# Kernel optimization log

Measured on AMD Instinct MI355X. Metric: run time of the kernel, lower is better.

The kernel has to match this reference:

```python
import jax, jax.numpy as jnp
import numpy as np

D_MODEL = 768
D_STATE = 16
D_CONV = 4
EXPAND = 2
D_IN = D_MODEL // 2          # per-direction model dim = 384
D_INNER = EXPAND * D_IN      # ssm inner dim = 768
DT_RANK = (D_IN + 15) // 16  # 24 (mamba 'auto')
B, L = 2, 2048
EPS = 1e-5


def silu(x):
    return x * jax.nn.sigmoid(x)


def layernorm(x, w, b):
    m = jnp.mean(x, axis=-1, keepdims=True)
    v = jnp.var(x, axis=-1, keepdims=True)
    return (x - m) * jax.lax.rsqrt(v + EPS) * w + b


def causal_conv1d(u, w, b):
    # u: (B,L,di), w: (di,K) depthwise causal conv, b: (di,)
    K = w.shape[1]
    up = jnp.pad(u, ((0, 0), (K - 1, 0), (0, 0)))
    Lq = u.shape[1]
    y = sum(up[:, k:k + Lq, :] * w[:, k] for k in range(K))
    return y + b


def mamba_ssm(u, in_w, in_b, conv_w, conv_b, xp_w, dt_w, dt_b, A_log, Dp, out_w, out_b):
    # u: (B,L,D_IN)
    Bz = u.shape[0]
    xz = u @ in_w + in_b                         # (B,L,2*D_INNER)
    x, z = jnp.split(xz, 2, axis=-1)             # (B,L,D_INNER) each
    x = silu(causal_conv1d(x, conv_w, conv_b))
    xd = x @ xp_w                                # (B,L,DT_RANK+2N)
    dt = jax.nn.softplus(xd[..., :DT_RANK] @ dt_w + dt_b)   # (B,L,D_INNER)
    Bm = xd[..., DT_RANK:DT_RANK + D_STATE]      # (B,L,N)
    Cm = xd[..., DT_RANK + D_STATE:]             # (B,L,N)
    A = -jnp.exp(A_log)                          # (D_INNER,N)

    def step(h, xs):
        dt_t, x_t, B_t, C_t = xs                 # (B,di),(B,di),(B,N),(B,N)
        h = jnp.exp(dt_t[..., None] * A) * h + (dt_t * x_t)[..., None] * B_t[:, None, :]
        y = jnp.einsum('bdn,bn->bd', h, C_t)
        return h, y

    h0 = jnp.zeros((Bz, D_INNER, D_STATE), x.dtype)
    xs = (dt.transpose(1, 0, 2), x.transpose(1, 0, 2),
          Bm.transpose(1, 0, 2), Cm.transpose(1, 0, 2))
    _, ys = jax.lax.scan(step, h0, xs)           # ys: (L,B,D_INNER)
    y = ys.transpose(1, 0, 2) + x * Dp
    y = y * silu(z)
    return y @ out_w + out_b                     # (B,L,D_IN)


def setup_inputs() -> dict:
    key = jax.random.key(0)

    def nrm(i, shape, s=0.02):
        return jax.random.normal(jax.random.fold_in(key, i), shape, jnp.float32) * s

    d = {"x": jax.random.normal(jax.random.fold_in(key, 0), (B, L, D_MODEL), jnp.float32)}
    d["in_norm_w"] = jnp.ones(D_MODEL); d["in_norm_b"] = jnp.zeros(D_MODEL)
    d["ip_w"] = nrm(1, (D_MODEL, 2 * D_IN)); d["ip_b"] = jnp.zeros(2 * D_IN)
    i = 10
    for p in ("f", "b"):
        d[p + "_in_w"] = nrm(i, (D_IN, 2 * D_INNER)); d[p + "_in_b"] = jnp.zeros(2 * D_INNER)
        d[p + "_conv_w"] = nrm(i + 1, (D_INNER, D_CONV), 0.2); d[p + "_conv_b"] = jnp.zeros(D_INNER)
        d[p + "_xp_w"] = nrm(i + 2, (D_INNER, DT_RANK + 2 * D_STATE))
        d[p + "_dt_w"] = nrm(i + 3, (DT_RANK, D_INNER), 0.1)
        d[p + "_dt_b"] = nrm(i + 4, (D_INNER,), 0.5)
        d[p + "_A_log"] = jnp.log(jnp.tile(jnp.arange(1, D_STATE + 1, dtype=jnp.float32), (D_INNER, 1)))
        d[p + "_D"] = jnp.ones(D_INNER)
        d[p + "_out_w"] = nrm(i + 5, (D_INNER, D_IN)); d[p + "_out_b"] = jnp.zeros(D_IN)
        i += 10
    d["op_w"] = nrm(30, (2 * D_IN, D_MODEL)); d["op_b"] = jnp.zeros(D_MODEL)
    d["norm_w"] = jnp.ones(D_MODEL); d["norm_b"] = jnp.zeros(D_MODEL)
    return d


def reference(x, in_norm_w, in_norm_b, ip_w, ip_b,
              f_in_w, f_in_b, f_conv_w, f_conv_b, f_xp_w, f_dt_w, f_dt_b, f_A_log, f_D, f_out_w, f_out_b,
              b_in_w, b_in_b, b_conv_w, b_conv_b, b_xp_w, b_dt_w, b_dt_b, b_A_log, b_D, b_out_w, b_out_b,
              op_w, op_b, norm_w, norm_b):
    residual = x
    xn = layernorm(x, in_norm_w, in_norm_b)
    xp = xn @ ip_w + ip_b                        # (B,L,2*D_IN)
    x_fwd, x_bwd = jnp.split(xp, 2, axis=-1)
    out_fwd = mamba_ssm(x_fwd, f_in_w, f_in_b, f_conv_w, f_conv_b, f_xp_w,
                        f_dt_w, f_dt_b, f_A_log, f_D, f_out_w, f_out_b)
    out_bwd = mamba_ssm(jnp.flip(x_bwd, axis=1), b_in_w, b_in_b, b_conv_w, b_conv_b, b_xp_w,
                        b_dt_w, b_dt_b, b_A_log, b_D, b_out_w, b_out_b)
    out_bwd = jnp.flip(out_bwd, axis=1)
    out = jnp.concatenate([out_fwd, out_bwd], axis=-1) @ op_w + op_b
    # dropout is identity in eval mode
    return layernorm(residual + out, norm_w, norm_b)
```

## Files before the change

### kernel.cpp

```cpp
#include <hip/hip_runtime.h>
#include <hip/hip_bf16.h>
#include <math.h>
#include <type_traits>

#define BATCH 2
#define SEQ   2048
#define DMODEL 768
#define DIN   384
#define DINNER 768
#define DSTATE 16
#define DTRANK 24
#define ROWS  (BATCH*SEQ)
#define NCH   32
#define CLEN  (SEQ/NCH)

using short8  = __attribute__((ext_vector_type(8))) short;
using floatx4 = __attribute__((ext_vector_type(4))) float;

__device__ __forceinline__ ushort f2bf(float f) {
    union { float f; uint u; } v; v.f = f;
    uint r = (v.u + 0x7fffu + ((v.u >> 16) & 1u)) >> 16;
    return (ushort)r;
}
__device__ __forceinline__ float bf2f(ushort h) {
    union { uint u; float f; } v; v.u = ((uint)h) << 16;
    return v.f;
}

__device__ __forceinline__ void async16(const ushort* g, ushort* l) {
    __builtin_amdgcn_global_load_lds(
        (const __attribute__((address_space(1))) void*)g,
        (__attribute__((address_space(3))) void*)l,
        16, 0, 0);
}

template<typename OUT>
__global__ __launch_bounds__(256) void ln_kernel(
    const float* __restrict__ x, const float* __restrict__ res,
    const float* __restrict__ w, const float* __restrict__ b,
    OUT* __restrict__ out)
{
    int row = blockIdx.x;
    int tid = threadIdx.x;
    const float* xr = x + (size_t)row * DMODEL;
    const float* rr = res ? res + (size_t)row * DMODEL : nullptr;
    float v[3];
    float s = 0.f, sq = 0.f;
#pragma unroll
    for (int j = 0; j < 3; j++) {
        int i = tid + j * 256;
        float val = xr[i];
        if (rr) val += rr[i];
        v[j] = val; s += val; sq += val * val;
    }
#pragma unroll
    for (int off = 32; off; off >>= 1) {
        s  += __shfl_down(s,  off);
        sq += __shfl_down(sq, off);
    }
    __shared__ float ss[4], ssq[4];
    __shared__ float mean_s, rstd_s;
    int wid = tid >> 6;
    if ((tid & 63) == 0) { ss[wid] = s; ssq[wid] = sq; }
    __syncthreads();
    if (tid == 0) {
        float S  = ss[0] + ss[1] + ss[2] + ss[3];
        float SQ = ssq[0] + ssq[1] + ssq[2] + ssq[3];
        float m  = S * (1.0f / DMODEL);
        float var = SQ * (1.0f / DMODEL) - m * m;
        mean_s = m;
        rstd_s = rsqrtf(var + 1e-5f);
    }
    __syncthreads();
    float m = mean_s, rs = rstd_s;
    OUT* orow = out + (size_t)row * DMODEL;
#pragma unroll
    for (int j = 0; j < 3; j++) {
        int i = tid + j * 256;
        float r = (v[j] - m) * rs * w[i] + b[i];
        if constexpr (std::is_same_v<OUT, ushort>) orow[i] = f2bf(r);
        else                                       orow[i] = r;
    }
}

struct TD { const float* src; ushort* dst; int K, N, Np, tile0, tk; };
struct TDs { TD d[8]; };

__global__ __launch_bounds__(256) void tcast_kernel(TDs ds)
{
    int bidx = blockIdx.x;
    int i = 0;
    while (i < 7 && bidx >= ds.d[i + 1].tile0) i++;
    TD t = ds.d[i];
    int local = bidx - t.tile0;
    int tk = local % t.tk, tn = local / t.tk;
    int tx = threadIdx.x & 31, ty = threadIdx.x >> 5;

    __shared__ float tile[32][33];
    int k0 = tk * 32, n0 = tn * 32;
#pragma unroll
    for (int r = ty; r < 32; r += 8) {
        int n = n0 + tx;
        tile[r][tx] = (n < t.N) ? t.src[(size_t)(k0 + r) * t.N + n] : 0.f;
    }
    __syncthreads();
#pragma unroll
    for (int r = ty; r < 32; r += 8) {
        int n = n0 + r, k = k0 + tx;
        t.dst[(size_t)n * t.K + k] = f2bf(tile[tx][r]);
    }
}

template<int TM, int TN, bool OUT_BF>
__global__ __launch_bounds__(256) void mfma_gemm(
    const ushort* __restrict__ A0, const ushort* __restrict__ A1, int lda,
    const ushort* __restrict__ B0, const ushort* __restrict__ B1, int ldb,
    const float* __restrict__ bias0, const float* __restrict__ bias1,
    void* __restrict__ C0, void* __restrict__ C1, int ldc, int N, int K)
{
    const ushort* A  = blockIdx.z ? A1 : A0;
    const ushort* Bt = blockIdx.z ? B1 : B0;
    const float* bias = blockIdx.z ? bias1 : bias0;
    void* Cout = blockIdx.z ? C1 : C0;

    constexpr int WM = TM / 2, WN = TN / 2;
    constexpr int MT = WM / 16, NT = WN / 16;
    __shared__ __align__(16) ushort lA[TM * 32];
    __shared__ __align__(16) ushort lB[TN * 32];
    const int tid = threadIdx.x;
    const int wave = tid >> 6, lane = tid & 63;
    const int wm = wave >> 1, wn = wave & 1;
    const int quad = lane >> 4, l16 = lane & 15;
    const int m0 = blockIdx.y * TM, n0 = blockIdx.x * TN;

    const int lrow = lane >> 2;
    const int lcol = (lane & 3) * 8;

    floatx4 acc[MT][NT];
#pragma unroll
    for (int i = 0; i < MT; i++)
#pragma unroll
        for (int j = 0; j < NT; j++)
            acc[i][j] = (floatx4){0.f, 0.f, 0.f, 0.f};

    constexpr int AI = TM / 64;
    constexpr int BI = TN / 64;

    for (int k0 = 0; k0 < K; k0 += 32) {
#pragma unroll
        for (int i = 0; i < AI; i++) {
            int rbase = (wave * AI + i) * 16;
            async16(A + (size_t)(m0 + rbase + lrow) * lda + k0 + lcol,
                    &lA[rbase * 32]);
        }
#pragma unroll
        for (int i = 0; i < BI; i++) {
            int rbase = (wave * BI + i) * 16;
            async16(Bt + (size_t)(n0 + rbase + lrow) * ldb + k0 + lcol,
                    &lB[rbase * 32]);
        }
        __syncthreads();
        short8 af[MT], bfr[NT];
#pragma unroll
        for (int i = 0; i < MT; i++)
            af[i] = *(const short8*)&lA[(wm * WM + i * 16 + l16) * 32 + quad * 8];
#pragma unroll
        for (int j = 0; j < NT; j++)
            bfr[j] = *(const short8*)&lB[(wn * WN + j * 16 + l16) * 32 + quad * 8];
#pragma unroll
        for (int i = 0; i < MT; i++)
#pragma unroll
            for (int j = 0; j < NT; j++)
                acc[i][j] = __builtin_amdgcn_mfma_f32_16x16x32_bf16(af[i], bfr[j], acc[i][j], 0, 0, 0);
        __syncthreads();
    }
#pragma unroll
    for (int i = 0; i < MT; i++) {
#pragma unroll
        for (int j = 0; j < NT; j++) {
            int row = m0 + wm * WM + i * 16 + quad * 4;
            int col = n0 + wn * WN + j * 16 + l16;
            if (col < N) {
                float bv = bias ? bias[col] : 0.f;
#pragma unroll
                for (int r = 0; r < 4; r++) {
                    float v = acc[i][j][r] + bv;
                    if (OUT_BF) ((ushort*)Cout)[(size_t)(row + r) * ldc + col] = f2bf(v);
                    else        ((float*)Cout)[(size_t)(row + r) * ldc + col] = v;
                }
            }
        }
    }
}

#define BM 64
#define BN 64
#define BK 16
__global__ __launch_bounds__(256) void dt_gemm_kernel(
    const float* __restrict__ A0f, const float* __restrict__ A1f, int lda,
    const float* __restrict__ W0, const float* __restrict__ W1, int ldw,
    const float* __restrict__ bias0, const float* __restrict__ bias1,
    float* __restrict__ C0f, float* __restrict__ C1f, int ldc,
    int M, int N, int K)
{
    const float* A = blockIdx.z ? A1f : A0f;
    const float* W = blockIdx.z ? W1 : W0;
    const float* bias = blockIdx.z ? bias1 : bias0;
    float* C = blockIdx.z ? C1f : C0f;

    __shared__ float As[BK][BM + 4];
    __shared__ float Bs[BK][BN + 4];
    int tid = threadIdx.x;
    int m0 = blockIdx.y * BM;
    int n0 = blockIdx.x * BN;
    int tx = tid & 15, ty = tid >> 4;
    float acc[4][4] = {};

    for (int k0 = 0; k0 < K; k0 += BK) {
        {
            int row = tid >> 2;
            int kq  = (tid & 3) * 4;
            const float* ap = A + (size_t)(m0 + row) * lda + k0 + kq;
            float4 av;
            if (k0 + BK <= K) {
                av = *(const float4*)ap;
            } else {
                float t0 = (k0 + kq + 0 < K) ? ap[0] : 0.f;
                float t1 = (k0 + kq + 1 < K) ? ap[1] : 0.f;
                float t2 = (k0 + kq + 2 < K) ? ap[2] : 0.f;
                float t3 = (k0 + kq + 3 < K) ? ap[3] : 0.f;
                av = make_float4(t0, t1, t2, t3);
            }
            As[kq + 0][row] = av.x;
            As[kq + 1][row] = av.y;
            As[kq + 2][row] = av.z;
            As[kq + 3][row] = av.w;
        }
        {
            int krow = tid >> 4;
            int col  = (tid & 15) * 4;
            float4 wv = make_float4(0.f, 0.f, 0.f, 0.f);
            if (k0 + krow < K) {
                const float* wp = W + (size_t)(k0 + krow) * ldw + n0 + col;
                wv = *(const float4*)wp;
            }
            *(float4*)&Bs[krow][col] = wv;
        }
        __syncthreads();
#pragma unroll
        for (int k = 0; k < BK; k++) {
            float a[4], bv[4];
            *(float4*)a  = *(const float4*)&As[k][ty * 4];
            *(float4*)bv = *(const float4*)&Bs[k][tx * 4];
#pragma unroll
            for (int i = 0; i < 4; i++)
#pragma unroll
                for (int j = 0; j < 4; j++)
                    acc[i][j] = fmaf(a[i], bv[j], acc[i][j]);
        }
        __syncthreads();
    }
#pragma unroll
    for (int i = 0; i < 4; i++) {
        int m = m0 + ty * 4 + i;
#pragma unroll
        for (int j = 0; j < 4; j++) {
            int n = n0 + tx * 4 + j;
            float v = acc[i][j] + bias[n];
            v = (v > 20.f) ? v : log1pf(__expf(v));
            C[(size_t)m * ldc + n] = v;
        }
    }
}

__global__ __launch_bounds__(256) void conv_silu_kernel(
    const ushort* __restrict__ xzf, const ushort* __restrict__ xzb,
    const float* __restrict__ cwf, const float* __restrict__ cbf,
    const float* __restrict__ cwb, const float* __restrict__ cbb,
    ushort* __restrict__ outf, ushort* __restrict__ outb)
{
    int rev = blockIdx.y;
    const ushort* xz = rev ? xzb : xzf;
    const float* cw = rev ? cwb : cwf;
    const float* cb = rev ? cbb : cbf;
    ushort* out = rev ? outb : outf;

    int idx = blockIdx.x * 256 + threadIdx.x;
    int d = idx % DINNER;
    int row = idx / DINNER;
    int t = row & (SEQ - 1);
    int b = row >> 11;
    float acc = cb[d];
#pragma unroll
    for (int k = 0; k < 4; k++) {
        int ts = rev ? (t + 3 - k) : (t - 3 + k);
        if (ts >= 0 && ts < SEQ)
            acc = fmaf(cw[d * 4 + k], bf2f(xz[((size_t)(b * SEQ + ts)) * 1536 + d]), acc);
    }
    float sig = 1.f / (1.f + __expf(-acc));
    out[idx] = f2bf(acc * sig);
}

template<bool FULL>
__global__ __launch_bounds__(256) void scan_chunk_kernel(
    const float* __restrict__ dtf, const ushort* __restrict__ xcf,
    const float* __restrict__ xdf, const ushort* __restrict__ xzf,
    const float* __restrict__ Alf, const float* __restrict__ Dff,
    const float* __restrict__ dtb, const ushort* __restrict__ xcb,
    const float* __restrict__ xdb, const ushort* __restrict__ xzb,
    const float* __restrict__ Alb, const float* __restrict__ Dbb,
    float* __restrict__ Hloc, float* __restrict__ Wp,
    const float* __restrict__ Hin,
    ushort* __restrict__ yf, ushort* __restrict__ yb)
{
    const int d     = blockIdx.x * 256 + threadIdx.x;
    const int chunk = blockIdx.y;
    const int bz    = blockIdx.z;
    const int dir   = bz >> 1;
    const int bat   = bz & 1;

    const float*  dt = dir ? dtb : dtf;
    const ushort* xc = dir ? xcb : xcf;
    const float*  xd = dir ? xdb : xdf;
    const ushort* xz = dir ? xzb : xzf;
    const float*  Al = dir ? Alb : Alf;
    const float*  Dp = dir ? Dbb : Dff;
    ushort* yo = dir ? yb : yf;

    float a[16];
    {
        const float4* Ap = (const float4*)(Al + (size_t)d * 16);
#pragma unroll
        for (int q = 0; q < 4; q++) {
            float4 v = Ap[q];
            a[q*4+0] = -__expf(v.x); a[q*4+1] = -__expf(v.y);
            a[q*4+2] = -__expf(v.z); a[q*4+3] = -__expf(v.w);
        }
    }
    const float a0 = a[0];
    bool fast = true;
#pragma unroll
    for (int n = 0; n < 16; n++) {
        float ideal = a0 * (float)(n + 1);
        fast = fast && (fabsf(a[n] - ideal) <= 1e-4f * fabsf(ideal) + 1e-7f);
    }

    float h[16];
    if (FULL) {
        size_t base = ((size_t)(bz * NCH + chunk) * DINNER + d) * 16;
        const float4* hp = (const float4*)(Hin + base);
#pragma unroll
        for (int q = 0; q < 4; q++) {
            float4 v = hp[q];
            h[q*4+0] = v.x; h[q*4+1] = v.y; h[q*4+2] = v.z; h[q*4+3] = v.w;
        }
    } else {
#pragma unroll
        for (int n = 0; n < 16; n++) h[n] = 0.f;
    }

    const float Dd = FULL ? Dp[d] : 0.f;
    float S = 0.f;

    auto run = [&](auto FASTC) {
        constexpr bool FAST = decltype(FASTC)::value;
#pragma unroll 2
        for (int i = 0; i < CLEN; i++) {
            int tl = chunk * CLEN + i;
            int t  = dir ? (SEQ - 1 - tl) : tl;
            size_t r = (size_t)(bat * SEQ + t);
            float dtv = dt[r * DINNER + d];
            float xv  = bf2f(xc[r * DINNER + d]);
            const float* bp = xd + r * 56 + DTRANK;
            float4 B0 = *(const float4*)(bp + 0);
            float4 B1 = *(const float4*)(bp + 4);
            float4 B2 = *(const float4*)(bp + 8);
            float4 B3 = *(const float4*)(bp + 12);
            float Bv[16] = {B0.x,B0.y,B0.z,B0.w, B1.x,B1.y,B1.z,B1.w,
                            B2.x,B2.y,B2.z,B2.w, B3.x,B3.y,B3.z,B3.w};
            float w[16];
            if (FAST) {
                float e1 = __expf(dtv * a0);
                float e2 = e1*e1, e4 = e2*e2, e8 = e4*e4;
                w[0]=e1;      w[1]=e2;      w[2]=e2*e1;   w[3]=e4;
                w[4]=e4*e1;   w[5]=e4*e2;   w[6]=e4*w[2]; w[7]=e8;
                w[8]=e8*e1;   w[9]=e8*e2;   w[10]=e8*w[2];w[11]=e8*e4;
                w[12]=e8*w[4];w[13]=e8*w[5];w[14]=e8*w[6];w[15]=e8*e8;
            } else {
#pragma unroll
                for (int n = 0; n < 16; n++) w[n] = __expf(dtv * a[n]);
            }
            float bx = dtv * xv;
#pragma unroll
            for (int n = 0; n < 16; n++)
                h[n] = fmaf(w[n], h[n], bx * Bv[n]);
            S += dtv;
            if (FULL) {
                const float* cp = bp + DSTATE;
                float4 C0 = *(const float4*)(cp + 0);
                float4 C1 = *(const float4*)(cp + 4);
                float4 C2 = *(const float4*)(cp + 8);
                float4 C3 = *(const float4*)(cp + 12);
                float Cv[16] = {C0.x,C0.y,C0.z,C0.w, C1.x,C1.y,C1.z,C1.w,
                                C2.x,C2.y,C2.z,C2.w, C3.x,C3.y,C3.z,C3.w};
                float y = 0.f;
#pragma unroll
                for (int n = 0; n < 16; n++) y = fmaf(h[n], Cv[n], y);
                float zv = bf2f(xz[r * 1536 + DINNER + d]);
                float sig = 1.f / (1.f + __expf(-zv));
                yo[r * DINNER + d] = f2bf((y + xv * Dd) * (zv * sig));
            }
        }
    };
    if (fast) run(std::true_type{}); else run(std::false_type{});

    if (!FULL) {
        float W[16];
        if (fast) {
            float E1 = __expf(S * a0);
            float E2 = E1*E1, E4 = E2*E2, E8 = E4*E4;
            W[0]=E1;      W[1]=E2;      W[2]=E2*E1;   W[3]=E4;
            W[4]=E4*E1;   W[5]=E4*E2;   W[6]=E4*W[2]; W[7]=E8;
            W[8]=E8*E1;   W[9]=E8*E2;   W[10]=E8*W[2];W[11]=E8*E4;
            W[12]=E8*W[4];W[13]=E8*W[5];W[14]=E8*W[6];W[15]=E8*E8;
        } else {
#pragma unroll
            for (int n = 0; n < 16; n++) W[n] = __expf(S * a[n]);
        }
        size_t base = ((size_t)(bz * NCH + chunk) * DINNER + d) * 16;
#pragma unroll
        for (int q = 0; q < 4; q++) {
            *(float4*)(Hloc + base + q*4) = make_float4(h[q*4+0], h[q*4+1], h[q*4+2], h[q*4+3]);
            *(float4*)(Wp   + base + q*4) = make_float4(W[q*4+0], W[q*4+1], W[q*4+2], W[q*4+3]);
        }
    }
}

__global__ __launch_bounds__(256) void scan_combine(
    const float* __restrict__ Hloc, const float* __restrict__ Wp,
    float* __restrict__ Hin)
{
    int idx = blockIdx.x * 256 + threadIdx.x;
    int bz = idx / (DINNER * 16);
    int rest = idx % (DINNER * 16);
    float hin = 0.f;
#pragma unroll
    for (int k = 0; k < NCH; k++) {
        size_t o = (size_t)(bz * NCH + k) * (DINNER * 16) + rest;
        Hin[o] = hin;
        hin = fmaf(Wp[o], hin, Hloc[o]);
    }
}

extern "C" void kernel_launch(void* const* d_in, const int* in_sizes, int n_in,
                              void* d_out, int out_size, void* d_ws, size_t ws_size,
                              hipStream_t stream)
{
    const float* x        = (const float*)d_in[0];
    const float* in_nw    = (const float*)d_in[1];
    const float* in_nb    = (const float*)d_in[2];
    const float* ip_w     = (const float*)d_in[3];
    const float* ip_b     = (const float*)d_in[4];
    const float* f_in_w   = (const float*)d_in[5];
    const float* f_in_b   = (const float*)d_in[6];
    const float* f_conv_w = (const float*)d_in[7];
    const float* f_conv_b = (const float*)d_in[8];
    const float* f_xp_w   = (const float*)d_in[9];
    const float* f_dt_w   = (const float*)d_in[10];
    const float* f_dt_b   = (const float*)d_in[11];
    const float* f_A_log  = (const float*)d_in[12];
    const float* f_D      = (const float*)d_in[13];
    const float* f_out_w  = (const float*)d_in[14];
    const float* f_out_b  = (const float*)d_in[15];
    const float* b_in_w   = (const float*)d_in[16];
    const float* b_in_b   = (const float*)d_in[17];
    const float* b_conv_w = (const float*)d_in[18];
    const float* b_conv_b = (const float*)d_in[19];
    const float* b_xp_w   = (const float*)d_in[20];
    const float* b_dt_w   = (const float*)d_in[21];
    const float* b_dt_b   = (const float*)d_in[22];
    const float* b_A_log  = (const float*)d_in[23];
    const float* b_D      = (const float*)d_in[24];
    const float* b_out_w  = (const float*)d_in[25];
    const float* b_out_b  = (const float*)d_in[26];
    const float* op_w     = (const float*)d_in[27];
    const float* op_b     = (const float*)d_in[28];
    const float* norm_w   = (const float*)d_in[29];
    const float* norm_b   = (const float*)d_in[30];

    size_t off = 0;
    auto alloc = [&](size_t bytes) {
        void* p = (char*)d_ws + off;
        off += (bytes + 255) & ~(size_t)255;
        return p;
    };
    const size_t R = ROWS;
    ushort* xn_bf   = (ushort*)alloc(R * 768 * 2);
    ushort* xp_bf   = (ushort*)alloc(R * 768 * 2);
    ushort* xz_f_bf = (ushort*)alloc(R * 1536 * 2);
    ushort* xz_b_bf = (ushort*)alloc(R * 1536 * 2);
    ushort* xc_f_bf = (ushort*)alloc(R * 768 * 2);
    ushort* xc_b_bf = (ushort*)alloc(R * 768 * 2);
    float*  xd_f    = (float*)alloc(R * 56 * 4);
    float*  xd_b    = (float*)alloc(R * 56 * 4);
    float*  dt_f    = (float*)alloc(R * 768 * 4);
    float*  dt_b    = (float*)alloc(R * 768 * 4);
    ushort* y_f_bf  = (ushort*)alloc(R * 768 * 2);
    ushort* y_b_bf  = (ushort*)alloc(R * 768 * 2);
    ushort* cat_bf  = (ushort*)alloc(R * 768 * 2);
    float*  outraw  = (float*)alloc(R * 768 * 4);
    const size_t SCN = (size_t)4 * NCH * DINNER * 16;
    float* Hloc = (float*)alloc(SCN * 4);
    float* Wpb  = (float*)alloc(SCN * 4);
    float* Hin  = (float*)alloc(SCN * 4);
    ushort* Wt_ip   = (ushort*)alloc((size_t)768 * 768 * 2);
    ushort* Wt_fin  = (ushort*)alloc((size_t)1536 * 384 * 2);
    ushort* Wt_bin  = (ushort*)alloc((size_t)1536 * 384 * 2);
    ushort* Wt_fxp  = (ushort*)alloc((size_t)64 * 768 * 2);
    ushort* Wt_bxp  = (ushort*)alloc((size_t)64 * 768 * 2);
    ushort* Wt_fout = (ushort*)alloc((size_t)384 * 768 * 2);
    ushort* Wt_bout = (ushort*)alloc((size_t)384 * 768 * 2);
    ushort* Wt_op   = (ushort*)alloc((size_t)768 * 768 * 2);

    dim3 blk(256);

    TDs td;
    int tile0 = 0, nd = 0;
    auto add = [&](const float* s, ushort* dst, int K, int N, int Np) {
        td.d[nd] = TD{s, dst, K, N, Np, tile0, K / 32};
        tile0 += (K / 32) * (Np / 32);
        nd++;
    };
    add(ip_w,    Wt_ip,   768, 768, 768);
    add(f_in_w,  Wt_fin,  384, 1536, 1536);
    add(b_in_w,  Wt_bin,  384, 1536, 1536);
    add(f_xp_w,  Wt_fxp,  768, 56, 64);
    add(b_xp_w,  Wt_bxp,  768, 56, 64);
    add(f_out_w, Wt_fout, 768, 384, 384);
    add(b_out_w, Wt_bout, 768, 384, 384);
    add(op_w,    Wt_op,   768, 768, 768);
    hipLaunchKernelGGL(tcast_kernel, dim3(tile0), blk, 0, stream, td);

    hipLaunchKernelGGL((ln_kernel<ushort>), dim3(ROWS), blk, 0, stream,
                       x, (const float*)nullptr, in_nw, in_nb, xn_bf);
    hipLaunchKernelGGL((mfma_gemm<128,64,true>), dim3(768/64, ROWS/128, 1), blk, 0, stream,
                       xn_bf, xn_bf, 768, Wt_ip, Wt_ip, 768, ip_b, ip_b,
                       (void*)xp_bf, (void*)xp_bf, 768, 768, 768);
    hipLaunchKernelGGL((mfma_gemm<128,128,true>), dim3(1536/128, ROWS/128, 2), blk, 0, stream,
                       xp_bf, xp_bf + 384, 768, Wt_fin, Wt_bin, 384,
                       f_in_b, b_in_b, (void*)xz_f_bf, (void*)xz_b_bf, 1536, 1536, 384);
    hipLaunchKernelGGL(conv_silu_kernel, dim3(ROWS * DINNER / 256, 2), blk, 0, stream,
                       xz_f_bf, xz_b_bf, f_conv_w, f_conv_b, b_conv_w, b_conv_b,
                       xc_f_bf, xc_b_bf);
    hipLaunchKernelGGL((mfma_gemm<64,64,false>), dim3(1, ROWS/64, 2), blk, 0, stream,
                       xc_f_bf, xc_b_bf, 768, Wt_fxp, Wt_bxp, 768,
                       (const float*)nullptr, (const float*)nullptr,
                       (void*)xd_f, (void*)xd_b, 56, 56, 768);
    hipLaunchKernelGGL(dt_gemm_kernel, dim3(768 / BN, ROWS / BM, 2), blk, 0, stream,
                       xd_f, xd_b, 56, f_dt_w, b_dt_w, 768, f_dt_b, b_dt_b,
                       dt_f, dt_b, 768, ROWS, 768, DTRANK);
    hipLaunchKernelGGL((scan_chunk_kernel<false>), dim3(DINNER / 256, NCH, 4), blk, 0, stream,
                       dt_f, xc_f_bf, xd_f, xz_f_bf, f_A_log, f_D,
                       dt_b, xc_b_bf, xd_b, xz_b_bf, b_A_log, b_D,
                       Hloc, Wpb, (const float*)nullptr, (ushort*)nullptr, (ushort*)nullptr);
    hipLaunchKernelGGL(scan_combine, dim3(4 * DINNER * 16 / 256), blk, 0, stream,
                       Hloc, Wpb, Hin);
    hipLaunchKernelGGL((scan_chunk_kernel<true>), dim3(DINNER / 256, NCH, 4), blk, 0, stream,
                       dt_f, xc_f_bf, xd_f, xz_f_bf, f_A_log, f_D,
                       dt_b, xc_b_bf, xd_b, xz_b_bf, b_A_log, b_D,
                       (float*)nullptr, (float*)nullptr, Hin, y_f_bf, y_b_bf);
    hipLaunchKernelGGL((mfma_gemm<128,64,true>), dim3(384/64, ROWS/128, 2), blk, 0, stream,
                       y_f_bf, y_b_bf, 768, Wt_fout, Wt_bout, 768,
                       f_out_b, b_out_b, (void*)cat_bf, (void*)(cat_bf + 384), 768, 384, 768);
    hipLaunchKernelGGL((mfma_gemm<128,64,false>), dim3(768/64, ROWS/128, 1), blk, 0, stream,
                       cat_bf, cat_bf, 768, Wt_op, Wt_op, 768, op_b, op_b,
                       (void*)outraw, (void*)outraw, 768, 768, 768);
    hipLaunchKernelGGL((ln_kernel<float>), dim3(ROWS), blk, 0, stream,
                       x, outraw, norm_w, norm_b, (float*)d_out);
}
```

Baseline: 352.3 us.

## Fold adjacent linear projections into fused weights and merge prep kernels

Precomputes combined weights by multiplying ip_w into the in_proj weights and the out_proj weights into op_w, with matching fused biases. The separate xp and cat GEMMs disappear and activations pass through fewer full-size matmuls and intermediate buffers. It also merges weight casting with the input layernorm into one launch, doubles the GEMM K-step to 64, vectorises the conv kernel to 8 channels per thread, and doubles the scan chunk count. The per-call weight-fusion GEMMs add cost, and rounding the fused weights to bf16 changes numerics slightly.

```diff
diff --git a/kernel.cpp b/kernel.cpp
--- a/kernel.cpp
+++ b/kernel.cpp
@@ -11,7 +11,7 @@
 #define DSTATE 16
 #define DTRANK 24
 #define ROWS  (BATCH*SEQ)
-#define NCH   32
+#define NCH   64
 #define CLEN  (SEQ/NCH)
 
 using short8  = __attribute__((ext_vector_type(8))) short;
@@ -26,7 +26,6 @@
     union { uint u; float f; } v; v.u = ((uint)h) << 16;
     return v.f;
 }
-
 __device__ __forceinline__ void async16(const ushort* g, ushort* l) {
     __builtin_amdgcn_global_load_lds(
         (const __attribute__((address_space(1))) void*)g,
@@ -34,13 +33,136 @@
         16, 0, 0);
 }
 
-template<typename OUT>
-__global__ __launch_bounds__(256) void ln_kernel(
-    const float* __restrict__ x, const float* __restrict__ res,
+template<int TM, int TN> struct GemmShT { ushort lA[TM * 64]; ushort lB[TN * 64]; };
+
+template<int TM, int TN>
+__device__ __forceinline__ void gemm_accum(
+    const ushort* __restrict__ A, int lda,
+    const ushort* __restrict__ Bt, int ldb,
+    int K, int m0, int n0, GemmShT<TM, TN>& sh,
+    floatx4 (&acc)[TM / 32][TN / 32])
+{
+    constexpr int WM = TM / 2, WN = TN / 2;
+    constexpr int MT = WM / 16, NT = WN / 16;
+    constexpr int AI = TM / 32, BI = TN / 32;
+    const int tid = threadIdx.x;
+    const int wave = tid >> 6, lane = tid & 63;
+    const int wm = wave >> 1, wn = wave & 1;
+    const int quad = lane >> 4, l16 = lane & 15;
+    const int lrow = lane >> 3, lcol = (lane & 7) * 8;
+
+    for (int k0 = 0; k0 < K; k0 += 64) {
+#pragma unroll
+        for (int i = 0; i < AI; i++) {
+            int rb = (wave * AI + i) * 8;
+            async16(A + (size_t)(m0 + rb + lrow) * lda + k0 + lcol, &sh.lA[rb * 64]);
+        }
+#pragma unroll
+        for (int i = 0; i < BI; i++) {
+            int rb = (wave * BI + i) * 8;
+            async16(Bt + (size_t)(n0 + rb + lrow) * ldb + k0 + lcol, &sh.lB[rb * 64]);
+        }
+        __syncthreads();
+#pragma unroll
+        for (int ks = 0; ks < 2; ks++) {
+            short8 af[MT], bf[NT];
+#pragma unroll
+            for (int i = 0; i < MT; i++)
+                af[i] = *(const short8*)&sh.lA[(wm * WM + i * 16 + l16) * 64 + ks * 32 + quad * 8];
+#pragma unroll
+            for (int j = 0; j < NT; j++)
+                bf[j] = *(const short8*)&sh.lB[(wn * WN + j * 16 + l16) * 64 + ks * 32 + quad * 8];
+#pragma unroll
+            for (int i = 0; i < MT; i++)
+#pragma unroll
+                for (int j = 0; j < NT; j++)
+                    acc[i][j] = __builtin_amdgcn_mfma_f32_16x16x32_bf16(af[i], bf[j], acc[i][j], 0, 0, 0);
+        }
+        __syncthreads();
+    }
+}
+
+template<int TM, int TN, bool OUT_BF>
+__device__ __forceinline__ void gemm_epilogue(
+    const float* __restrict__ bias, void* __restrict__ C, int ldc, int N,
+    int m0, int n0, floatx4 (&acc)[TM / 32][TN / 32])
+{
+    constexpr int WM = TM / 2, WN = TN / 2;
+    constexpr int MT = WM / 16, NT = WN / 16;
+    const int tid = threadIdx.x;
+    const int wave = tid >> 6, lane = tid & 63;
+    const int wm = wave >> 1, wn = wave & 1;
+    const int quad = lane >> 4, l16 = lane & 15;
+#pragma unroll
+    for (int i = 0; i < MT; i++) {
+#pragma unroll
+        for (int j = 0; j < NT; j++) {
+            int row = m0 + wm * WM + i * 16 + quad * 4;
+            int col = n0 + wn * WN + j * 16 + l16;
+            if (col < N) {
+                float bv = bias ? bias[col] : 0.f;
+#pragma unroll
+                for (int r = 0; r < 4; r++) {
+                    float v = acc[i][j][r] + bv;
+                    if (OUT_BF) ((ushort*)C)[(size_t)(row + r) * ldc + col] = f2bf(v);
+                    else        ((float*)C)[(size_t)(row + r) * ldc + col] = v;
+                }
+            }
+        }
+    }
+}
+
+template<int TM, int TN, bool OUT_BF>
+__global__ __launch_bounds__(256) void mfma_gemm_k(
+    const ushort* __restrict__ A0, const ushort* __restrict__ A1, int lda,
+    const ushort* __restrict__ B0, const ushort* __restrict__ B1, int ldb,
+    const float* __restrict__ bias0, const float* __restrict__ bias1,
+    void* __restrict__ C0, void* __restrict__ C1, int ldc, int N, int K)
+{
+    __shared__ GemmShT<TM, TN> sh;
+    const ushort* A  = blockIdx.z ? A1 : A0;
+    const ushort* Bt = blockIdx.z ? B1 : B0;
+    const float* bias = blockIdx.z ? bias1 : bias0;
+    void* C = blockIdx.z ? C1 : C0;
+    floatx4 acc[TM / 32][TN / 32];
+#pragma unroll
+    for (int i = 0; i < TM / 32; i++)
+#pragma unroll
+        for (int j = 0; j < TN / 32; j++)
+            acc[i][j] = (floatx4){0.f, 0.f, 0.f, 0.f};
+    int m0 = blockIdx.y * TM, n0 = blockIdx.x * TN;
+    gemm_accum<TM, TN>(A, lda, Bt, ldb, K, m0, n0, sh, acc);
+    gemm_epilogue<TM, TN, OUT_BF>(bias, C, ldc, N, m0, n0, acc);
+}
+
+template<int TM, int TN>
+__global__ __launch_bounds__(256) void outop_kernel(
+    const ushort* __restrict__ A0, const ushort* __restrict__ B0,
+    const ushort* __restrict__ A1, const ushort* __restrict__ B1,
+    const float* __restrict__ bias, float* __restrict__ C,
+    int lda, int ldb, int ldc, int N, int K)
+{
+    __shared__ GemmShT<TM, TN> sh;
+    floatx4 acc[TM / 32][TN / 32];
+#pragma unroll
+    for (int i = 0; i < TM / 32; i++)
+#pragma unroll
+        for (int j = 0; j < TN / 32; j++)
+            acc[i][j] = (floatx4){0.f, 0.f, 0.f, 0.f};
+    int m0 = blockIdx.y * TM, n0 = blockIdx.x * TN;
+    gemm_accum<TM, TN>(A0, lda, B0, ldb, K, m0, n0, sh, acc);
+    gemm_accum<TM, TN>(A1, lda, B1, ldb, K, m0, n0, sh, acc);
+    gemm_epilogue<TM, TN, false>(bias, (void*)C, ldc, N, m0, n0, acc);
+}
+
+struct LnSh { float ss[4]; float ssq[4]; float m; float rs; };
+
+template<bool OUT_BF>
+__device__ __forceinline__ void ln_row(
+    int row, const float* __restrict__ x, const float* __restrict__ res,
     const float* __restrict__ w, const float* __restrict__ b,
-    OUT* __restrict__ out)
-{
-    int row = blockIdx.x;
+    void* __restrict__ out, LnSh& sh)
+{
     int tid = threadIdx.x;
     const float* xr = x + (size_t)row * DMODEL;
     const float* rr = res ? res + (size_t)row * DMODEL : nullptr;
@@ -58,139 +180,169 @@
         s  += __shfl_down(s,  off);
         sq += __shfl_down(sq, off);
     }
-    __shared__ float ss[4], ssq[4];
-    __shared__ float mean_s, rstd_s;
     int wid = tid >> 6;
-    if ((tid & 63) == 0) { ss[wid] = s; ssq[wid] = sq; }
+    if ((tid & 63) == 0) { sh.ss[wid] = s; sh.ssq[wid] = sq; }
     __syncthreads();
     if (tid == 0) {
-        float S  = ss[0] + ss[1] + ss[2] + ss[3];
-        float SQ = ssq[0] + ssq[1] + ssq[2] + ssq[3];
+        float S  = sh.ss[0] + sh.ss[1] + sh.ss[2] + sh.ss[3];
+        float SQ = sh.ssq[0] + sh.ssq[1] + sh.ssq[2] + sh.ssq[3];
         float m  = S * (1.0f / DMODEL);
         float var = SQ * (1.0f / DMODEL) - m * m;
-        mean_s = m;
-        rstd_s = rsqrtf(var + 1e-5f);
+        sh.m = m;
+        sh.rs = rsqrtf(var + 1e-5f);
     }
     __syncthreads();
-    float m = mean_s, rs = rstd_s;
-    OUT* orow = out + (size_t)row * DMODEL;
+    float m = sh.m, rs = sh.rs;
 #pragma unroll
     for (int j = 0; j < 3; j++) {
         int i = tid + j * 256;
         float r = (v[j] - m) * rs * w[i] + b[i];
-        if constexpr (std::is_same_v<OUT, ushort>) orow[i] = f2bf(r);
-        else                                       orow[i] = r;
-    }
-}
-
-struct TD { const float* src; ushort* dst; int K, N, Np, tile0, tk; };
-struct TDs { TD d[8]; };
-
-__global__ __launch_bounds__(256) void tcast_kernel(TDs ds)
-{
-    int bidx = blockIdx.x;
-    int i = 0;
-    while (i < 7 && bidx >= ds.d[i + 1].tile0) i++;
-    TD t = ds.d[i];
-    int local = bidx - t.tile0;
-    int tk = local % t.tk, tn = local / t.tk;
-    int tx = threadIdx.x & 31, ty = threadIdx.x >> 5;
-
-    __shared__ float tile[32][33];
-    int k0 = tk * 32, n0 = tn * 32;
-#pragma unroll
-    for (int r = ty; r < 32; r += 8) {
-        int n = n0 + tx;
-        tile[r][tx] = (n < t.N) ? t.src[(size_t)(k0 + r) * t.N + n] : 0.f;
-    }
-    __syncthreads();
-#pragma unroll
-    for (int r = ty; r < 32; r += 8) {
-        int n = n0 + r, k = k0 + tx;
-        t.dst[(size_t)n * t.K + k] = f2bf(tile[tx][r]);
-    }
-}
-
-template<int TM, int TN, bool OUT_BF>
-__global__ __launch_bounds__(256) void mfma_gemm(
-    const ushort* __restrict__ A0, const ushort* __restrict__ A1, int lda,
-    const ushort* __restrict__ B0, const ushort* __restrict__ B1, int ldb,
-    const float* __restrict__ bias0, const float* __restrict__ bias1,
-    void* __restrict__ C0, void* __restrict__ C1, int ldc, int N, int K)
-{
-    const ushort* A  = blockIdx.z ? A1 : A0;
-    const ushort* Bt = blockIdx.z ? B1 : B0;
-    const float* bias = blockIdx.z ? bias1 : bias0;
-    void* Cout = blockIdx.z ? C1 : C0;
-
-    constexpr int WM = TM / 2, WN = TN / 2;
-    constexpr int MT = WM / 16, NT = WN / 16;
-    __shared__ __align__(16) ushort lA[TM * 32];
-    __shared__ __align__(16) ushort lB[TN * 32];
-    const int tid = threadIdx.x;
-    const int wave = tid >> 6, lane = tid & 63;
-    const int wm = wave >> 1, wn = wave & 1;
-    const int quad = lane >> 4, l16 = lane & 15;
-    const int m0 = blockIdx.y * TM, n0 = blockIdx.x * TN;
-
-    const int lrow = lane >> 2;
-    const int lcol = (lane & 3) * 8;
-
-    floatx4 acc[MT][NT];
-#pragma unroll
-    for (int i = 0; i < MT; i++)
-#pragma unroll
-        for (int j = 0; j < NT; j++)
-            acc[i][j] = (floatx4){0.f, 0.f, 0.f, 0.f};
-
-    constexpr int AI = TM / 64;
-    constexpr int BI = TN / 64;
-
-    for (int k0 = 0; k0 < K; k0 += 32) {
-#pragma unroll
-        for (int i = 0; i < AI; i++) {
-            int rbase = (wave * AI + i) * 16;
-            async16(A + (size_t)(m0 + rbase + lrow) * lda + k0 + lcol,
-                    &lA[rbase * 32]);
-        }
-#pragma unroll
-        for (int i = 0; i < BI; i++) {
-            int rbase = (wave * BI + i) * 16;
-            async16(Bt + (size_t)(n0 + rbase + lrow) * ldb + k0 + lcol,
-                    &lB[rbase * 32]);
-        }
-        __syncthreads();
-        short8 af[MT], bfr[NT];
-#pragma unroll
-        for (int i = 0; i < MT; i++)
-            af[i] = *(const short8*)&lA[(wm * WM + i * 16 + l16) * 32 + quad * 8];
-#pragma unroll
-        for (int j = 0; j < NT; j++)
-            bfr[j] = *(const short8*)&lB[(wn * WN + j * 16 + l16) * 32 + quad * 8];
-#pragma unroll
-        for (int i = 0; i < MT; i++)
-#pragma unroll
-            for (int j = 0; j < NT; j++)
-                acc[i][j] = __builtin_amdgcn_mfma_f32_16x16x32_bf16(af[i], bfr[j], acc[i][j], 0, 0, 0);
-        __syncthreads();
-    }
-#pragma unroll
-    for (int i = 0; i < MT; i++) {
-#pragma unroll
-        for (int j = 0; j < NT; j++) {
-            int row = m0 + wm * WM + i * 16 + quad * 4;
-            int col = n0 + wn * WN + j * 16 + l16;
-            if (col < N) {
-                float bv = bias ? bias[col] : 0.f;
-#pragma unroll
-                for (int r = 0; r < 4; r++) {
-                    float v = acc[i][j][r] + bv;
-                    if (OUT_BF) ((ushort*)Cout)[(size_t)(row + r) * ldc + col] = f2bf(v);
-                    else        ((float*)Cout)[(size_t)(row + r) * ldc + col] = v;
-                }
+        if (OUT_BF) ((ushort*)out)[(size_t)row * DMODEL + i] = f2bf(r);
+        else        ((float*)out)[(size_t)row * DMODEL + i] = r;
+    }
+}
+
+__global__ __launch_bounds__(256) void ln2_kernel(
+    const float* __restrict__ x, const float* __restrict__ res,
+    const float* __restrict__ w, const float* __restrict__ b,
+    float* __restrict__ out)
+{
+    __shared__ LnSh sh;
+    ln_row<false>(blockIdx.x, x, res, w, b, (void*)out, sh);
+}
+
+struct TD { const float* src; ushort* dst; int K, N, Np, tile0, tk, mode; };
+struct PrepArgs {
+    TD d[8];
+    int ntc;
+    const float *x, *in_nw, *in_nb;
+    ushort* xn;
+};
+
+__global__ __launch_bounds__(256) void prep_kernel(PrepArgs p)
+{
+    __shared__ union { float tile[32][33]; LnSh l; } sh;
+    int bi = blockIdx.x;
+    if (bi < p.ntc) {
+        int i = 0;
+        while (i < 7 && bi >= p.d[i + 1].tile0) i++;
+        TD t = p.d[i];
+        int local = bi - t.tile0;
+        int tki = local % t.tk, tn = local / t.tk;
+        int k0 = tki * 32, n0 = tn * 32;
+        if (t.mode == 0) {
+            int tx = threadIdx.x & 31, ty = threadIdx.x >> 5;
+#pragma unroll
+            for (int r = ty; r < 32; r += 8) {
+                int n = n0 + tx;
+                sh.tile[r][tx] = (n < t.N) ? t.src[(size_t)(k0 + r) * t.N + n] : 0.f;
             }
-        }
-    }
+            __syncthreads();
+#pragma unroll
+            for (int r = ty; r < 32; r += 8) {
+                int n = n0 + r, k = k0 + tx;
+                t.dst[(size_t)n * t.K + k] = f2bf(sh.tile[tx][r]);
+            }
+        } else {
+#pragma unroll
+            for (int e = threadIdx.x; e < 1024; e += 256) {
+                int r = e >> 5, c = e & 31;
+                size_t o = (size_t)(k0 + r) * t.N + n0 + c;
+                t.dst[o] = f2bf(t.src[o]);
+            }
+        }
+    } else {
+        ln_row<true>(bi - p.ntc, p.x, (const float*)nullptr, p.in_nw, p.in_nb,
+                     (void*)p.xn, sh.l);
+    }
+}
+
+struct WfArgs {
+    const ushort *fin, *bin, *opT, *ipc, *fow, *bow;
+    ushort *WzF, *WzB, *WoF, *WoB;
+    const float *ip_b, *f_in_b, *b_in_b, *f_out_b, *b_out_b, *op_b;
+    const float *f_in_w32, *b_in_w32, *op_w32;
+    float *bzf, *bzb, *bo;
+};
+
+__global__ __launch_bounds__(256) void wfuse_kernel(WfArgs p)
+{
+    __shared__ GemmShT<128, 64> sh;
+    int t = blockIdx.x;
+    if (t < 432) {
+        const ushort *A, *Bt; ushort* C; int lda, ldb, m0, n0;
+        if (t < 144)      { A = p.fin;       lda = 384; Bt = p.ipc;       ldb = 768; C = p.WzF; int u = t;       m0 = (u / 12) * 128; n0 = (u % 12) * 64; }
+        else if (t < 288) { A = p.bin;       lda = 384; Bt = p.ipc + 384; ldb = 768; C = p.WzB; int u = t - 144; m0 = (u / 12) * 128; n0 = (u % 12) * 64; }
+        else if (t < 360) { A = p.opT;       lda = 768; Bt = p.fow;       ldb = 384; C = p.WoF; int u = t - 288; m0 = (u / 12) * 128; n0 = (u % 12) * 64; }
+        else              { A = p.opT + 384; lda = 768; Bt = p.bow;       ldb = 384; C = p.WoB; int u = t - 360; m0 = (u / 12) * 128; n0 = (u % 12) * 64; }
+        floatx4 acc[4][2];
+#pragma unroll
+        for (int i = 0; i < 4; i++)
+#pragma unroll
+            for (int j = 0; j < 2; j++)
+                acc[i][j] = (floatx4){0.f, 0.f, 0.f, 0.f};
+        gemm_accum<128, 64>(A, lda, Bt, ldb, 384, m0, n0, sh, acc);
+        gemm_epilogue<128, 64, true>((const float*)nullptr, (void*)C, 768, 768, m0, n0, acc);
+    } else if (t < 438) {
+        int n = (t - 432) * 256 + threadIdx.x;
+        float acc = p.f_in_b[n];
+        for (int j = 0; j < 384; j++)
+            acc = fmaf(p.ip_b[j], p.f_in_w32[(size_t)j * 1536 + n], acc);
+        p.bzf[n] = acc;
+    } else if (t < 444) {
+        int n = (t - 438) * 256 + threadIdx.x;
+        float acc = p.b_in_b[n];
+        for (int j = 0; j < 384; j++)
+            acc = fmaf(p.ip_b[384 + j], p.b_in_w32[(size_t)j * 1536 + n], acc);
+        p.bzb[n] = acc;
+    } else {
+        int n = (t - 444) * 256 + threadIdx.x;
+        float acc = p.op_b[n];
+        for (int j = 0; j < 384; j++)
+            acc = fmaf(p.f_out_b[j], p.op_w32[(size_t)j * 768 + n], acc);
+        for (int j = 0; j < 384; j++)
+            acc = fmaf(p.b_out_b[j], p.op_w32[(size_t)(384 + j) * 768 + n], acc);
+        p.bo[n] = acc;
+    }
+}
+
+__global__ __launch_bounds__(256) void conv_silu_kernel(
+    const ushort* __restrict__ xzf, const ushort* __restrict__ xzb,
+    const float* __restrict__ cwf, const float* __restrict__ cbf,
+    const float* __restrict__ cwb, const float* __restrict__ cbb,
+    ushort* __restrict__ outf, ushort* __restrict__ outb)
+{
+    int rev = blockIdx.y;
+    const ushort* xz = rev ? xzb : xzf;
+    const float* cw = rev ? cwb : cwf;
+    const float* cb = rev ? cbb : cbf;
+    ushort* out = rev ? outb : outf;
+
+    int idx = blockIdx.x * 256 + threadIdx.x;
+    int dg = idx % (DINNER / 8);
+    int row = idx / (DINNER / 8);
+    int d0 = dg * 8;
+    int t = row & (SEQ - 1), b = row >> 11;
+    float acc[8];
+#pragma unroll
+    for (int c = 0; c < 8; c++) acc[c] = cb[d0 + c];
+#pragma unroll
+    for (int k = 0; k < 4; k++) {
+        int ts = rev ? (t + 3 - k) : (t - 3 + k);
+        if (ts >= 0 && ts < SEQ) {
+            short8 v = *(const short8*)&xz[((size_t)(b * SEQ + ts)) * 1536 + d0];
+#pragma unroll
+            for (int c = 0; c < 8; c++)
+                acc[c] = fmaf(cw[(d0 + c) * 4 + k], bf2f((ushort)v[c]), acc[c]);
+        }
+    }
+    short8 o;
+#pragma unroll
+    for (int c = 0; c < 8; c++) {
+        float sig = 1.f / (1.f + __expf(-acc[c]));
+        o[c] = (short)f2bf(acc[c] * sig);
+    }
+    *(short8*)&out[(size_t)row * DINNER + d0] = o;
 }
 
 #define BM 64
@@ -200,8 +352,7 @@
     const float* __restrict__ A0f, const float* __restrict__ A1f, int lda,
     const float* __restrict__ W0, const float* __restrict__ W1, int ldw,
     const float* __restrict__ bias0, const float* __restrict__ bias1,
-    float* __restrict__ C0f, float* __restrict__ C1f, int ldc,
-    int M, int N, int K)
+    float* __restrict__ C0f, float* __restrict__ C1f, int ldc, int K)
 {
     const float* A = blockIdx.z ? A1f : A0f;
     const float* W = blockIdx.z ? W1 : W0;
@@ -221,29 +372,17 @@
             int row = tid >> 2;
             int kq  = (tid & 3) * 4;
             const float* ap = A + (size_t)(m0 + row) * lda + k0 + kq;
-            float4 av;
-            if (k0 + BK <= K) {
-                av = *(const float4*)ap;
-            } else {
-                float t0 = (k0 + kq + 0 < K) ? ap[0] : 0.f;
-                float t1 = (k0 + kq + 1 < K) ? ap[1] : 0.f;
-                float t2 = (k0 + kq + 2 < K) ? ap[2] : 0.f;
-                float t3 = (k0 + kq + 3 < K) ? ap[3] : 0.f;
-                av = make_float4(t0, t1, t2, t3);
-            }
-            As[kq + 0][row] = av.x;
-            As[kq + 1][row] = av.y;
-            As[kq + 2][row] = av.z;
-            As[kq + 3][row] = av.w;
+            As[kq + 0][row] = (k0 + kq + 0 < K) ? ap[0] : 0.f;
+            As[kq + 1][row] = (k0 + kq + 1 < K) ? ap[1] : 0.f;
+            As[kq + 2][row] = (k0 + kq + 2 < K) ? ap[2] : 0.f;
+            As[kq + 3][row] = (k0 + kq + 3 < K) ? ap[3] : 0.f;
         }
         {
             int krow = tid >> 4;
             int col  = (tid & 15) * 4;
             float4 wv = make_float4(0.f, 0.f, 0.f, 0.f);
-            if (k0 + krow < K) {
-                const float* wp = W + (size_t)(k0 + krow) * ldw + n0 + col;
-                wv = *(const float4*)wp;
-            }
+            if (k0 + krow < K)
+                wv = *(const float4*)(W + (size_t)(k0 + krow) * ldw + n0 + col);
             *(float4*)&Bs[krow][col] = wv;
         }
         __syncthreads();
@@ -271,34 +410,6 @@
             C[(size_t)m * ldc + n] = v;
         }
     }
-}
-
-__global__ __launch_bounds__(256) void conv_silu_kernel(
-    const ushort* __restrict__ xzf, const ushort* __restrict__ xzb,
-    const float* __restrict__ cwf, const float* __restrict__ cbf,
-    const float* __restrict__ cwb, const float* __restrict__ cbb,
-    ushort* __restrict__ outf, ushort* __restrict__ outb)
-{
-    int rev = blockIdx.y;
-    const ushort* xz = rev ? xzb : xzf;
-    const float* cw = rev ? cwb : cwf;
-    const float* cb = rev ? cbb : cbf;
-    ushort* out = rev ? outb : outf;
-
-    int idx = blockIdx.x * 256 + threadIdx.x;
-    int d = idx % DINNER;
-    int row = idx / DINNER;
-    int t = row & (SEQ - 1);
-    int b = row >> 11;
-    float acc = cb[d];
-#pragma unroll
-    for (int k = 0; k < 4; k++) {
-        int ts = rev ? (t + 3 - k) : (t - 3 + k);
-        if (ts >= 0 && ts < SEQ)
-            acc = fmaf(cw[d * 4 + k], bf2f(xz[((size_t)(b * SEQ + ts)) * 1536 + d]), acc);
-    }
-    float sig = 1.f / (1.f + __expf(-acc));
-    out[idx] = f2bf(acc * sig);
 }
 
 template<bool FULL>
@@ -348,10 +459,9 @@
     float h[16];
     if (FULL) {
         size_t base = ((size_t)(bz * NCH + chunk) * DINNER + d) * 16;
-        const float4* hp = (const float4*)(Hin + base);
 #pragma unroll
         for (int q = 0; q < 4; q++) {
-            float4 v = hp[q];
+            float4 v = *(const float4*)(Hin + base + q * 4);
             h[q*4+0] = v.x; h[q*4+1] = v.y; h[q*4+2] = v.z; h[q*4+3] = v.w;
         }
     } else {
@@ -444,7 +554,7 @@
     int bz = idx / (DINNER * 16);
     int rest = idx % (DINNER * 16);
     float hin = 0.f;
-#pragma unroll
+#pragma unroll 4
     for (int k = 0; k < NCH; k++) {
         size_t o = (size_t)(bz * NCH + k) * (DINNER * 16) + rest;
         Hin[o] = hin;
@@ -496,7 +606,6 @@
     };
     const size_t R = ROWS;
     ushort* xn_bf   = (ushort*)alloc(R * 768 * 2);
-    ushort* xp_bf   = (ushort*)alloc(R * 768 * 2);
     ushort* xz_f_bf = (ushort*)alloc(R * 1536 * 2);
     ushort* xz_b_bf = (ushort*)alloc(R * 1536 * 2);
     ushort* xc_f_bf = (ushort*)alloc(R * 768 * 2);
@@ -507,74 +616,88 @@
     float*  dt_b    = (float*)alloc(R * 768 * 4);
     ushort* y_f_bf  = (ushort*)alloc(R * 768 * 2);
     ushort* y_b_bf  = (ushort*)alloc(R * 768 * 2);
-    ushort* cat_bf  = (ushort*)alloc(R * 768 * 2);
     float*  outraw  = (float*)alloc(R * 768 * 4);
     const size_t SCN = (size_t)4 * NCH * DINNER * 16;
     float* Hloc = (float*)alloc(SCN * 4);
     float* Wpb  = (float*)alloc(SCN * 4);
     float* Hin  = (float*)alloc(SCN * 4);
-    ushort* Wt_ip   = (ushort*)alloc((size_t)768 * 768 * 2);
-    ushort* Wt_fin  = (ushort*)alloc((size_t)1536 * 384 * 2);
-    ushort* Wt_bin  = (ushort*)alloc((size_t)1536 * 384 * 2);
-    ushort* Wt_fxp  = (ushort*)alloc((size_t)64 * 768 * 2);
-    ushort* Wt_bxp  = (ushort*)alloc((size_t)64 * 768 * 2);
-    ushort* Wt_fout = (ushort*)alloc((size_t)384 * 768 * 2);
-    ushort* Wt_bout = (ushort*)alloc((size_t)384 * 768 * 2);
-    ushort* Wt_op   = (ushort*)alloc((size_t)768 * 768 * 2);
-
-    dim3 blk(256);
-
-    TDs td;
+    ushort* Wt_fin = (ushort*)alloc((size_t)1536 * 384 * 2);
+    ushort* Wt_bin = (ushort*)alloc((size_t)1536 * 384 * 2);
+    ushort* Wt_op  = (ushort*)alloc((size_t)768 * 768 * 2);
+    ushort* Wt_fxp = (ushort*)alloc((size_t)64 * 768 * 2);
+    ushort* Wt_bxp = (ushort*)alloc((size_t)64 * 768 * 2);
+    ushort* ipc    = (ushort*)alloc((size_t)768 * 768 * 2);
+    ushort* fow    = (ushort*)alloc((size_t)768 * 384 * 2);
+    ushort* bow    = (ushort*)alloc((size_t)768 * 384 * 2);
+    ushort* WzF    = (ushort*)alloc((size_t)1536 * 768 * 2);
+    ushort* WzB    = (ushort*)alloc((size_t)1536 * 768 * 2);
+    ushort* WoF    = (ushort*)alloc((size_t)768 * 768 * 2);
+    ushort* WoB    = (ushort*)alloc((size_t)768 * 768 * 2);
+    float*  bzf    = (float*)alloc(1536 * 4);
+    float*  bzb    = (float*)alloc(1536 * 4);
+    float*  bo     = (float*)alloc(768 * 4);
+
+    PrepArgs pa;
     int tile0 = 0, nd = 0;
-    auto add = [&](const float* s, ushort* dst, int K, int N, int Np) {
-        td.d[nd] = TD{s, dst, K, N, Np, tile0, K / 32};
-        tile0 += (K / 32) * (Np / 32);
+    auto add = [&](const float* s, ushort* dst, int K, int N, int Np, int mode) {
+        int tiles = mode == 0 ? (K / 32) * (Np / 32) : (K / 32) * (N / 32);
+        pa.d[nd] = TD{s, dst, K, N, Np, tile0, K / 32, mode};
+        tile0 += tiles;
         nd++;
     };
-    add(ip_w,    Wt_ip,   768, 768, 768);
-    add(f_in_w,  Wt_fin,  384, 1536, 1536);
-    add(b_in_w,  Wt_bin,  384, 1536, 1536);
-    add(f_xp_w,  Wt_fxp,  768, 56, 64);
-    add(b_xp_w,  Wt_bxp,  768, 56, 64);
-    add(f_out_w, Wt_fout, 768, 384, 384);
-    add(b_out_w, Wt_bout, 768, 384, 384);
-    add(op_w,    Wt_op,   768, 768, 768);
-    hipLaunchKernelGGL(tcast_kernel, dim3(tile0), blk, 0, stream, td);
-
-    hipLaunchKernelGGL((ln_kernel<ushort>), dim3(ROWS), blk, 0, stream,
-                       x, (const float*)nullptr, in_nw, in_nb, xn_bf);
-    hipLaunchKernelGGL((mfma_gemm<128,64,true>), dim3(768/64, ROWS/128, 1), blk, 0, stream,
-                       xn_bf, xn_bf, 768, Wt_ip, Wt_ip, 768, ip_b, ip_b,
-                       (void*)xp_bf, (void*)xp_bf, 768, 768, 768);
-    hipLaunchKernelGGL((mfma_gemm<128,128,true>), dim3(1536/128, ROWS/128, 2), blk, 0, stream,
-                       xp_bf, xp_bf + 384, 768, Wt_fin, Wt_bin, 384,
-                       f_in_b, b_in_b, (void*)xz_f_bf, (void*)xz_b_bf, 1536, 1536, 384);
-    hipLaunchKernelGGL(conv_silu_kernel, dim3(ROWS * DINNER / 256, 2), blk, 0, stream,
+    add(f_in_w,  Wt_fin, 384, 1536, 1536, 0);
+    add(b_in_w,  Wt_bin, 384, 1536, 1536, 0);
+    add(op_w,    Wt_op,  768, 768, 768, 0);
+    add(f_xp_w,  Wt_fxp, 768, 56, 64, 0);
+    add(b_xp_w,  Wt_bxp, 768, 56, 64, 0);
+    add(ip_w,    ipc,    768, 768, 768, 1);
+    add(f_out_w, fow,    768, 384, 384, 1);
+    add(b_out_w, bow,    768, 384, 384, 1);
+    pa.ntc = tile0;
+    pa.x = x; pa.in_nw = in_nw; pa.in_nb = in_nb; pa.xn = xn_bf;
+    hipLaunchKernelGGL(prep_kernel, dim3(tile0 + ROWS), dim3(256), 0, stream, pa);
+
+    WfArgs wa;
+    wa.fin = Wt_fin; wa.bin = Wt_bin; wa.opT = Wt_op;
+    wa.ipc = ipc; wa.fow = fow; wa.bow = bow;
+    wa.WzF = WzF; wa.WzB = WzB; wa.WoF = WoF; wa.WoB = WoB;
+    wa.ip_b = ip_b; wa.f_in_b = f_in_b; wa.b_in_b = b_in_b;
+    wa.f_out_b = f_out_b; wa.b_out_b = b_out_b; wa.op_b = op_b;
+    wa.f_in_w32 = f_in_w; wa.b_in_w32 = b_in_w; wa.op_w32 = op_w;
+    wa.bzf = bzf; wa.bzb = bzb; wa.bo = bo;
+    hipLaunchKernelGGL(wfuse_kernel, dim3(447), dim3(256), 0, stream, wa);
+
+    hipLaunchKernelGGL((mfma_gemm_k<128, 128, true>), dim3(12, 32, 2), dim3(256), 0, stream,
+                       xn_bf, xn_bf, 768, WzF, WzB, 768, bzf, bzb,
+                       (void*)xz_f_bf, (void*)xz_b_bf, 1536, 1536, 768);
+
+    hipLaunchKernelGGL(conv_silu_kernel, dim3(ROWS * DINNER / 8 / 256, 2), dim3(256), 0, stream,
                        xz_f_bf, xz_b_bf, f_conv_w, f_conv_b, b_conv_w, b_conv_b,
                        xc_f_bf, xc_b_bf);
-    hipLaunchKernelGGL((mfma_gemm<64,64,false>), dim3(1, ROWS/64, 2), blk, 0, stream,
+
+    hipLaunchKernelGGL((mfma_gemm_k<128, 64, false>), dim3(1, 32, 2), dim3(256), 0, stream,
                        xc_f_bf, xc_b_bf, 768, Wt_fxp, Wt_bxp, 768,
                        (const float*)nullptr, (const float*)nullptr,
                        (void*)xd_f, (void*)xd_b, 56, 56, 768);
-    hipLaunchKernelGGL(dt_gemm_kernel, dim3(768 / BN, ROWS / BM, 2), blk, 0, stream,
+
+    hipLaunchKernelGGL(dt_gemm_kernel, dim3(768 / BN, ROWS / BM, 2), dim3(256), 0, stream,
                        xd_f, xd_b, 56, f_dt_w, b_dt_w, 768, f_dt_b, b_dt_b,
-                       dt_f, dt_b, 768, ROWS, 768, DTRANK);
-    hipLaunchKernelGGL((scan_chunk_kernel<false>), dim3(DINNER / 256, NCH, 4), blk, 0, stream,
+                       dt_f, dt_b, 768, DTRANK);
+
+    hipLaunchKernelGGL((scan_chunk_kernel<false>), dim3(DINNER / 256, NCH, 4), dim3(256), 0, stream,
                        dt_f, xc_f_bf, xd_f, xz_f_bf, f_A_log, f_D,
                        dt_b, xc_b_bf, xd_b, xz_b_bf, b_A_log, b_D,
                        Hloc, Wpb, (const float*)nullptr, (ushort*)nullptr, (ushort*)nullptr);
-    hipLaunchKernelGGL(scan_combine, dim3(4 * DINNER * 16 / 256), blk, 0, stream,
+    hipLaunchKernelGGL(scan_combine, dim3(4 * DINNER * 16 / 256), dim3(256), 0, stream,
                        Hloc, Wpb, Hin);
-    hipLaunchKernelGGL((scan_chunk_kernel<true>), dim3(DINNER / 256, NCH, 4), blk, 0, stream,
+    hipLaunchKernelGGL((scan_chunk_kernel<true>), dim3(DINNER / 256, NCH, 4), dim3(256), 0, stream,
                        dt_f, xc_f_bf, xd_f, xz_f_bf, f_A_log, f_D,
                        dt_b, xc_b_bf, xd_b, xz_b_bf, b_A_log, b_D,
                        (float*)nullptr, (float*)nullptr, Hin, y_f_bf, y_b_bf);
-    hipLaunchKernelGGL((mfma_gemm<128,64,true>), dim3(384/64, ROWS/128, 2), blk, 0, stream,
-                       y_f_bf, y_b_bf, 768, Wt_fout, Wt_bout, 768,
-                       f_out_b, b_out_b, (void*)cat_bf, (void*)(cat_bf + 384), 768, 384, 768);
-    hipLaunchKernelGGL((mfma_gemm<128,64,false>), dim3(768/64, ROWS/128, 1), blk, 0, stream,
-                       cat_bf, cat_bf, 768, Wt_op, Wt_op, 768, op_b, op_b,
-                       (void*)outraw, (void*)outraw, 768, 768, 768);
-    hipLaunchKernelGGL((ln_kernel<float>), dim3(ROWS), blk, 0, stream,
+
+    hipLaunchKernelGGL((outop_kernel<128, 64>), dim3(12, 32), dim3(256), 0, stream,
+                       y_f_bf, WoF, y_b_bf, WoB, bo, outraw, 768, 768, 768, 768, 768);
+
+    hipLaunchKernelGGL(ln2_kernel, dim3(ROWS), dim3(256), 0, stream,
                        x, outraw, norm_w, norm_b, (float*)d_out);
 }
```

Measured after the change: 401.7 us. 1.14x slower.
